# Kernel optimization log

Measured on AMD Instinct MI355X. Metric: run time of the kernel, lower is better.

## Reference

```python
import jax, jax.numpy as jnp
from jax import lax
import numpy as np

M, CLS, K, DL, DC, DO, BD = 87, 65, 128, 128, 128, 2048, 256
B, H, W = 256, 7, 7


def _c1(x, Wt, b):
    # 1x1 Conv2d: [B,Cin,H,W] -> [B,Cout,H,W]
    return jnp.einsum('oc,bchw->bohw', Wt, x) + b[None, :, None, None]


def _pagerank(edge, v_init, p=0.85, iters=100):
    # torch: transition = adj / adj.sum(dim=1)  (broadcast divides COLUMNS by row-sums)
    n = edge.shape[0]
    Wpr = p * edge / jnp.sum(edge, axis=1)[None, :]
    s = v_init * n                                  # [B,n,1]
    coef = (1.0 - p) / n
    def body(i, xv):
        zx = coef * jnp.sum(xv, axis=1, keepdims=True)      # z_T @ x -> [B,1,1]
        return jnp.einsum('ij,bjo->bio', Wpr, xv) + s * zx
    xv = lax.fori_loop(0, iters, body, s)
    nrm = jnp.sqrt(jnp.sum(xv * xv, axis=1, keepdims=True))  # F.normalize(dim=1)
    xv = xv / jnp.maximum(nrm, 1e-12)
    return (v_init + xv).reshape(v_init.shape[0], -1)        # [B,n]


def setup_inputs() -> dict:
    key = jax.random.key(0)
    ks = jax.random.split(key, 24)
    def w(k, shape, s=0.02):
        return jax.random.normal(k, shape, jnp.float32) * s
    rng = np.random.default_rng(0)
    A = (rng.random((M, M)) < 0.08).astype(np.float32)
    A = np.maximum(A, A.T)
    np.fill_diagonal(A, 1.0)   # symmetric adjacency with self-loops (degrees > 0)
    return {
        'x': jax.random.normal(ks[0], (B, DO, H, W), jnp.float32),
        'Wb': w(ks[1], (BD, DO)), 'bb': w(ks[2], (BD,), 0.01),
        'Wfc': w(ks[3], (CLS, BD)), 'Wfc2': w(ks[4], (CLS, BD)),
        'Wo1': w(ks[5], (4 * DL, DO)), 'bo1': w(ks[6], (4 * DL,), 0.01),
        'Wo2': w(ks[7], (DL, 4 * DL)), 'bo2': w(ks[8], (DL,), 0.01),
        'Wa': w(ks[9], (M, DL)), 'ba': w(ks[10], (M,), 0.01),
        'Wps': w(ks[11], (DC, DL)), 'bps': w(ks[12], (DC,), 0.01),
        'node_p': jax.random.uniform(ks[13], (K, M), jnp.float32, -0.1, 0.1),
        'Wg': w(ks[14], (DC, DC + K)), 'bg': w(ks[15], (DC,), 0.01),
        'Wsp': w(ks[16], (DL, DC)), 'bsp': w(ks[17], (DL,), 0.01),
        'Ws': w(ks[18], (1, DC + DL)), 'bs': w(ks[19], (1,), 0.01),
        'Wox1': w(ks[20], (4 * DL, DL)), 'box1': w(ks[21], (4 * DL,), 0.01),
        'Wox2': w(ks[22], (DO, 4 * DL)), 'box2': w(ks[23], (DO,), 0.01),
        'edge': jnp.asarray(A),
    }


def reference(x, Wb, bb, Wfc, Wfc2, Wo1, bo1, Wo2, bo2, Wa, ba, Wps, bps,
              node_p, Wg, bg, Wsp, bsp, Ws, bs, Wox1, box1, Wox2, box2, edge):
    Bsz, _, hl, wl = x.shape
    HW = hl * wl

    # global pooled branch
    x_p = jnp.mean(x, axis=(2, 3))                           # [B,2048]
    features_p = x_p @ Wb.T + bb                             # [B,256]
    pre_output = features_p @ Wfc.T                          # [B,65]
    pre_score = jax.nn.softmax(lax.stop_gradient(pre_output), axis=1)

    # personalized pagerank over the semantic graph (constant wrt grads)
    v_init = jnp.concatenate(
        [jnp.zeros((Bsz, M - CLS), x.dtype), pre_score], axis=1)[:, :, None]
    v_y = lax.stop_gradient(_pagerank(edge, v_init))         # [B,87]

    # local feature reduction 2048 -> 512 -> 128
    x_l = _c1(_c1(x, Wo1, bo1), Wo2, bo2)                    # [B,128,7,7]

    a = _c1(x_l, Wa, ba).reshape(Bsz, M, HW).transpose(0, 2, 1)   # [B,HW,87]
    ps = _c1(x_l, Wps, bps).reshape(Bsz, DC, HW)                  # [B,128,HW]
    m1 = jax.nn.relu(jnp.matmul(ps, a))                           # [B,128,87]

    # replicate torch's exact (k, B*m) reshape + flat v_y broadcast
    node = jnp.broadcast_to(node_p[None], (Bsz, K, M)).reshape(K, Bsz * M)
    node = (v_y.reshape(-1) * node).reshape(Bsz, K, M)

    g = jnp.einsum('oc,bcm->bom', Wg, jnp.concatenate([node, m1], axis=1)) \
        + bg[None, :, None]                                   # [B,128,87]

    # D^-1/2 A D^-1/2 graph propagation
    Dinv = jnp.sum(edge, axis=0) ** -0.5
    edge_norm = Dinv[:, None] * edge * Dinv[None, :]
    m2 = jax.nn.relu(jnp.einsum('bcm,mn->bcn', g, edge_norm))  # [B,128,87]

    sp = jnp.einsum('oc,bcm->bom', Wsp, m2) + bsp[None, :, None]  # [B,128,87]

    # conv_s over concat(m2_expand, x_expand) is separable: avoid the
    # [B,256,HW,87] tensor entirely (1 output channel, 1x1 kernel).
    Ws1, Ws2 = Ws[0, :DC], Ws[0, DC:]
    t_node = jnp.einsum('c,bcm->bm', Ws1, m2)                  # [B,87]
    t_pix = jnp.einsum('c,bcp->bp', Ws2, x_l.reshape(Bsz, DL, HW))  # [B,HW]
    s_logits = t_node[:, :, None] + t_pix[:, None, :] + bs[0]  # [B,87,HW]
    s_att = jax.nn.softmax(s_logits, axis=1)                   # softmax over nodes

    m3 = jax.nn.relu(jnp.matmul(sp, s_att)).reshape(Bsz, DL, hl, wl)
    m3 = _c1(_c1(m3, Wox1, box1), Wox2, box2)                  # [B,2048,7,7]

    feature_aug = jnp.mean(m3, axis=(2, 3)) @ Wb.T + bb
    features = features_p + feature_aug
    outputs2 = features @ Wfc2.T
    softmax_outputs = jax.nn.softmax(outputs2, axis=1)
    return (features, outputs2, softmax_outputs, pre_output, features_p)
```

## Files before the change

### kernel.cpp

```cpp
#include <hip/hip_runtime.h>
#include <cmath>


typedef __attribute__((ext_vector_type(8))) short short8;
typedef __attribute__((ext_vector_type(4))) short s16x4;
typedef __attribute__((ext_vector_type(4))) float f32x4;

constexpr size_t OFF_W12BF = 0;
constexpr size_t OFF_T1BF  = 131072;
constexpr size_t OFF_WBBF  = 262144;
constexpr size_t OFF_XPBF  = 524288;
constexpr size_t OFF_WAPBF = 786432;
constexpr size_t OFF_WG2BF = 800768;
constexpr size_t OFF_ENPBF = 808960;
constexpr size_t OFF_B215  = 813568;
constexpr size_t OFF_B12   = 813792;
constexpr size_t OFF_WPR   = 813920;
constexpr size_t OFF_BTMP  = 821496;
constexpr size_t OFF_WC    = 823544;
constexpr size_t OFF_BC    = 856312;
constexpr size_t OFF_VY    = 856568;
constexpr size_t OFF_NT    = 878848;
constexpr size_t OFF_PART  = 901376;

__device__ __forceinline__ unsigned short f2bf(float f) {
  unsigned u = __builtin_bit_cast(unsigned, f);
  u += 0x7fffu + ((u >> 16) & 1u);
  return (unsigned short)(u >> 16);
}
__device__ __forceinline__ float bf2f(unsigned short s) {
  return __builtin_bit_cast(float, ((unsigned)s) << 16);
}

__global__ __launch_bounds__(256) void ksetup_all(
    const float* __restrict__ Wb,  const float* __restrict__ bb,
    const float* __restrict__ Wa,  const float* __restrict__ ba,
    const float* __restrict__ Wps, const float* __restrict__ bps,
    const float* __restrict__ Wg,  const float* __restrict__ edge,
    const float* __restrict__ Wo2, const float* __restrict__ Wo1,
    const float* __restrict__ Wox2,const float* __restrict__ Wox1,
    const float* __restrict__ box1,const float* __restrict__ box2,
    const float* __restrict__ bo1, const float* __restrict__ bo2,
    float* __restrict__ ws, float* __restrict__ featp)
{
  __shared__ alignas(16) short As[64*72];
  __shared__ alignas(16) short Bs[64*72];
  int blk = blockIdx.x, tid = threadIdx.x;
  if (blk < 2048) {
    int idx = blk*256 + tid;
    ((unsigned short*)(ws+OFF_WBBF))[idx] = f2bf(Wb[idx]);
  } else if (blk < 2304) {
    int idx = (blk-2048)*256 + tid;
    featp[idx] = bb[idx & 255];
  } else if (blk < 2432) {
    int idx = (blk-2304)*256 + tid;
    ws[OFF_WC + idx] = 0.f;
  } else if (blk < 2544) {
    int idx = (blk-2432)*256 + tid;
    int r = idx >> 7, c = idx & 127;
    float v;
    if (r < 128)      v = Wps[r*128 + c];
    else if (r < 215) v = Wa[(r-128)*128 + c];
    else              v = 0.f;
    ((unsigned short*)(ws+OFF_WAPBF))[idx] = f2bf(v);
  } else if (blk < 2608) {
    int idx = (blk-2544)*256 + tid;
    int o = idx >> 7, d = idx & 127;
    ((unsigned short*)(ws+OFF_WG2BF))[idx] = f2bf(Wg[o*256 + 128 + d]);
  } else if (blk < 2644) {
    int idx = (blk-2608)*256 + tid;
    int m = idx / 96, n = idx % 96;
    float v = 0.f;
    if (m < 87 && n < 87) {
      float sm = 0.f, sn = 0.f;
      for (int k = 0; k < 87; ++k) { sm += edge[k*87+m]; sn += edge[k*87+n]; }
      v = edge[m*87+n] / sqrtf(sm*sn);
    }
    ((unsigned short*)(ws+OFF_ENPBF))[idx] = f2bf(v);
  } else if (blk < 2674) {
    int idx = (blk-2644)*256 + tid;
    if (idx < 87*87) {
      int j = idx % 87;
      float rs = 0.f;
      for (int k = 0; k < 87; ++k) rs += edge[j*87+k];
      ws[OFF_WPR + idx] = 0.85f * edge[idx] / rs;
    }
  } else if (blk == 2674) {
    if (tid < 224) {
      float v = (tid < 128) ? bps[tid] : (tid < 215 ? ba[tid-128] : 0.f);
      ws[OFF_B215 + tid] = v;
    }
  } else if (blk < 2803) {
    int gb = blk - 2675;
    const float *A, *B; unsigned short* C; int lda, ldb, ldc, i0, j0;
    if (gb < 64) {
      A = Wo2; B = Wo1; C = (unsigned short*)(ws+OFF_W12BF);
      lda = 512; ldb = 2048; ldc = 2048;
      i0 = (gb & 1)*64; j0 = (gb >> 1)*64;
    } else {
      int b2 = gb - 64;
      A = Wox2; B = Wox1; C = (unsigned short*)(ws+OFF_T1BF);
      lda = 512; ldb = 128; ldc = 128;
      i0 = (b2 >> 1)*64; j0 = (b2 & 1)*64;
    }
    int w = tid >> 6, l = tid & 63, quad = l >> 4, lane16 = l & 15;
    f32x4 acc[4];
    #pragma unroll
    for (int i = 0; i < 4; ++i) acc[i] = (f32x4)(0.f);
    for (int kc = 0; kc < 512; kc += 64) {
      for (int t = tid; t < 1024; t += 256) {
        int r = t >> 4, k4 = t & 15;
        float4 v = *(const float4*)&A[(size_t)(i0+r)*lda + kc + k4*4];
        s16x4 sv; sv[0]=(short)f2bf(v.x); sv[1]=(short)f2bf(v.y); sv[2]=(short)f2bf(v.z); sv[3]=(short)f2bf(v.w);
        *(s16x4*)&As[r*72 + k4*4] = sv;
      }
      for (int t = tid; t < 1024; t += 256) {
        int kr = t >> 4, n4 = t & 15;
        float4 v = *(const float4*)&B[(size_t)(kc+kr)*ldb + j0 + n4*4];
        Bs[(n4*4+0)*72 + kr] = (short)f2bf(v.x);
        Bs[(n4*4+1)*72 + kr] = (short)f2bf(v.y);
        Bs[(n4*4+2)*72 + kr] = (short)f2bf(v.z);
        Bs[(n4*4+3)*72 + kr] = (short)f2bf(v.w);
      }
      __syncthreads();
      #pragma unroll
      for (int ks = 0; ks < 2; ++ks) {
        short8 a = *(const short8*)&As[(w*16+lane16)*72 + ks*32 + quad*8];
        #pragma unroll
        for (int nt = 0; nt < 4; ++nt) {
          short8 b8 = *(const short8*)&Bs[(nt*16+lane16)*72 + ks*32 + quad*8];
          acc[nt] = __builtin_amdgcn_mfma_f32_16x16x32_bf16(a, b8, acc[nt], 0, 0, 0);
        }
      }
      __syncthreads();
    }
    #pragma unroll
    for (int nt = 0; nt < 4; ++nt)
      #pragma unroll
      for (int r = 0; r < 4; ++r)
        C[(size_t)(i0 + w*16 + quad*4 + r)*ldc + j0 + nt*16 + lane16] = f2bf(acc[nt][r]);
  } else {
    int vb = blk - 2803;
    int w = tid >> 6, l = tid & 63;
    if (vb < 512) {
      int o = vb*4 + w;
      float s = 0.f;
      for (int h = l; h < 512; h += 64) s += Wox2[(size_t)o*512 + h] * box1[h];
      for (int off = 32; off; off >>= 1) s += __shfl_down(s, off, 64);
      if (l == 0) ws[OFF_BTMP + o] = s + box2[o];
    } else {
      int o = (vb - 512)*4 + w;
      float s = 0.f;
      for (int h = l; h < 512; h += 64) s += Wo2[(size_t)o*512 + h] * bo1[h];
      for (int off = 32; off; off >>= 1) s += __shfl_down(s, off, 64);
      if (l == 0) ws[OFF_B12 + o] = s + bo2[o];
    }
  }
}

__global__ __launch_bounds__(256) void kwcbc(const float* __restrict__ Wb,
                                             const float* __restrict__ bb,
                                             float* __restrict__ ws)
{
  __shared__ alignas(16) short As[64*72];
  __shared__ alignas(16) short Bs[64*72];
  int blk = blockIdx.x, tid = threadIdx.x;
  if (blk < 64) {
    const short* wbbf = (const short*)(ws+OFF_WBBF);
    const short* t1s  = (const short*)(ws+OFF_T1BF);
    int i0 = (blk & 3)*64, j0 = ((blk >> 2) & 1)*64, kc0 = (blk >> 3)*256;
    int w = tid >> 6, l = tid & 63, quad = l >> 4, lane16 = l & 15;
    f32x4 acc[4];
    #pragma unroll
    for (int i = 0; i < 4; ++i) acc[i] = (f32x4)(0.f);
    for (int kc = kc0; kc < kc0+256; kc += 64) {
      for (int t = tid; t < 512; t += 256) {
        int r = t >> 3, c8 = t & 7;
        *(short8*)&As[r*72 + c8*8] = *(const short8*)&wbbf[(size_t)(i0+r)*2048 + kc + c8*8];
      }
      for (int t = tid; t < 1024; t += 256) {
        int kr = t >> 4, n4 = t & 15;
        s16x4 v = *(const s16x4*)&t1s[(size_t)(kc+kr)*128 + j0 + n4*4];
        Bs[(n4*4+0)*72 + kr] = v[0];
        Bs[(n4*4+1)*72 + kr] = v[1];
        Bs[(n4*4+2)*72 + kr] = v[2];
        Bs[(n4*4+3)*72 + kr] = v[3];
      }
      __syncthreads();
      #pragma unroll
      for (int ks = 0; ks < 2; ++ks) {
        short8 a = *(const short8*)&As[(w*16+lane16)*72 + ks*32 + quad*8];
        #pragma unroll
        for (int nt = 0; nt < 4; ++nt) {
          short8 b8 = *(const short8*)&Bs[(nt*16+lane16)*72 + ks*32 + quad*8];
          acc[nt] = __builtin_amdgcn_mfma_f32_16x16x32_bf16(a, b8, acc[nt], 0, 0, 0);
        }
      }
      __syncthreads();
    }
    #pragma unroll
    for (int nt = 0; nt < 4; ++nt)
      #pragma unroll
      for (int r = 0; r < 4; ++r)
        atomicAdd(&ws[OFF_WC + (size_t)(i0 + w*16 + quad*4 + r)*128 + j0 + nt*16 + lane16], acc[nt][r]);
  } else {
    int j = (blk-64)*4 + (tid >> 6), l = tid & 63;
    float s = 0.f;
    for (int c = l; c < 2048; c += 64) s += Wb[(size_t)j*2048 + c] * ws[OFF_BTMP + c];
    for (int off = 32; off; off >>= 1) s += __shfl_down(s, off, 64);
    if (l == 0) ws[OFF_BC + j] = s + bb[j];
  }
}

__global__ __launch_bounds__(512) void kmain4(const float* __restrict__ x,
                                              const short* __restrict__ w12bf,
                                              short* __restrict__ xpbf,
                                              float* __restrict__ part)
{
  __shared__ alignas(16) short Bt[2][52*72];
  int b = blockIdx.x, half = blockIdx.y, tid = threadIdx.x;
  int w = tid >> 6, l = tid & 63;
  int quad = l >> 4, lane16 = l & 15;
  const float* xb = x + ((size_t)b*2048 + half*1024)*49;

  int p0 = tid % 49, oct0 = tid / 49;
  bool has0 = (tid < 392);

  float g0[8];
  if (has0) {
    #pragma unroll
    for (int j = 0; j < 8; ++j) g0[j] = xb[(size_t)(oct0*8+j)*49 + p0];
  }

  f32x4 acc[4];
  #pragma unroll
  for (int i = 0; i < 4; ++i) acc[i] = (f32x4)(0.f);

  for (int kci = 0; kci < 16; ++kci) {
    int kc = kci*64;
    short* bt = Bt[kci & 1];
    if (has0) {
      short8 v;
      #pragma unroll
      for (int j = 0; j < 8; ++j) v[j] = (short)f2bf(g0[j]);
      *(short8*)(bt + p0*72 + oct0*8) = v;
    }
    __syncthreads();
    if (kci < 15 && has0) {
      const float* xc = xb + (size_t)(kc+64)*49;
      #pragma unroll
      for (int j = 0; j < 8; ++j) g0[j] = xc[(size_t)(oct0*8+j)*49 + p0];
    }
    const short* wr = w12bf + (size_t)(w*16 + lane16)*2048 + half*1024 + kc + quad*8;
    short8 a0 = *(const short8*)(wr);
    short8 a1 = *(const short8*)(wr + 32);
    #pragma unroll
    for (int ni = 0; ni < 4; ++ni) {
      const short* br = bt + (ni*16 + lane16)*72 + quad*8;
      short8 b0 = *(const short8*)(br);
      short8 b1 = *(const short8*)(br + 32);
      acc[ni] = __builtin_amdgcn_mfma_f32_16x16x32_bf16(a0, b0, acc[ni], 0, 0, 0);
      acc[ni] = __builtin_amdgcn_mfma_f32_16x16x32_bf16(a1, b1, acc[ni], 0, 0, 0);
    }
    if (tid < 64) {
      float s = 0.f;
      for (int p = 0; p < 49; ++p)
        s += bf2f((unsigned short)bt[p*72 + tid]);
      xpbf[(size_t)b*2048 + half*1024 + kc + tid] = (short)f2bf(s * (1.f/49.f));
    }
  }
  float* po = part + ((size_t)half*256 + b)*128*52;
  #pragma unroll
  for (int ni = 0; ni < 4; ++ni) {
    int p = ni*16 + lane16;
    if (p < 49) {
      #pragma unroll
      for (int r = 0; r < 4; ++r) {
        int o = w*16 + quad*4 + r;
        po[o*52 + p] = acc[ni][r];
      }
    }
  }
}

__global__ __launch_bounds__(256) void kfeat(const short* __restrict__ xpbf,
                                             const short* __restrict__ wbbf,
                                             float* __restrict__ featp)
{
  int i0 = blockIdx.x*64, j0 = blockIdx.y*64, kc0 = blockIdx.z*256;
  int tid = threadIdx.x, w = tid >> 6, l = tid & 63, quad = l >> 4, lane16 = l & 15;
  f32x4 acc[4];
  #pragma unroll
  for (int i = 0; i < 4; ++i) acc[i] = (f32x4)(0.f);
  for (int kc = kc0; kc < kc0+256; kc += 32) {
    short8 a = *(const short8*)&xpbf[(size_t)(i0 + w*16 + lane16)*2048 + kc + quad*8];
    #pragma unroll
    for (int nt = 0; nt < 4; ++nt) {
      short8 b8 = *(const short8*)&wbbf[(size_t)(j0 + nt*16 + lane16)*2048 + kc + quad*8];
      acc[nt] = __builtin_amdgcn_mfma_f32_16x16x32_bf16(a, b8, acc[nt], 0, 0, 0);
    }
  }
  #pragma unroll
  for (int nt = 0; nt < 4; ++nt)
    #pragma unroll
    for (int r = 0; r < 4; ++r)
      atomicAdd(&featp[(size_t)(i0 + w*16 + quad*4 + r)*256 + j0 + nt*16 + lane16], acc[nt][r]);
}

__global__ __launch_bounds__(128, 1) void kpr(const float* __restrict__ featp,
                                              const float* __restrict__ Wfc,
                                              const float* __restrict__ wpr,
                                              float* __restrict__ preo,
                                              float* __restrict__ vy)
{
  __shared__ alignas(16) float fpr[256];
  __shared__ alignas(16) float po[68];
  __shared__ alignas(16) float vs[2][88];
  __shared__ float red[2];
  int b = blockIdx.x, tid = threadIdx.x;
  fpr[tid] = featp[b*256 + tid];
  fpr[tid+128] = featp[b*256 + 128 + tid];
  __syncthreads();
  if (tid < 65) {
    float s = 0.f;
    for (int c = 0; c < 256; c += 4) {
      float4 w4 = *(const float4*)&Wfc[tid*256 + c];
      s += w4.x*fpr[c] + w4.y*fpr[c+1] + w4.z*fpr[c+2] + w4.w*fpr[c+3];
    }
    po[tid] = s;
    preo[b*65 + tid] = s;
  }
  __syncthreads();
  if (tid < 64) {
    float v = po[tid];
    if (tid == 0) v = fmaxf(v, po[64]);
    float mx = v;
    #pragma unroll
    for (int off = 32; off; off >>= 1) mx = fmaxf(mx, __shfl_down(mx, off, 64));
    mx = __shfl(mx, 0, 64);
    float e = expf(po[tid]-mx) + ((tid == 0) ? expf(po[64]-mx) : 0.f);
    float sm = e;
    #pragma unroll
    for (int off = 32; off; off >>= 1) sm += __shfl_down(sm, off, 64);
    if (tid == 0) { red[0] = mx; red[1] = 1.f/sm; }
  }
  __syncthreads();
  float vinit = 0.f;
  if (tid >= 22 && tid < 87) vinit = expf(po[tid-22]-red[0]) * red[1];
  float s_i = vinit * 87.f;
  float wrow[87];
  if (tid < 87) {
    float add = s_i * (0.15f/87.0f);
    #pragma unroll
    for (int j = 0; j < 87; ++j) wrow[j] = wpr[tid*87 + j] + add;
    vs[0][tid] = s_i;
  }
  __syncthreads();
  for (int it = 0; it < 64; ++it) {
    const float* vc = vs[it & 1];
    if (tid < 87) {
      float nv = 0.f;
      #pragma unroll
      for (int j4 = 0; j4 < 21; ++j4) {
        float4 v4 = *(const float4*)&vc[j4*4];
        nv += wrow[j4*4+0]*v4.x + wrow[j4*4+1]*v4.y + wrow[j4*4+2]*v4.z + wrow[j4*4+3]*v4.w;
      }
      nv += wrow[84]*vc[84] + wrow[85]*vc[85] + wrow[86]*vc[86];
      vs[(it+1) & 1][tid] = nv;
    }
    __syncthreads();
  }
  if (tid < 64) {
    float v = vs[0][tid]*vs[0][tid];
    if (tid < 23) v += vs[0][64+tid]*vs[0][64+tid];
    #pragma unroll
    for (int off = 32; off; off >>= 1) v += __shfl_down(v, off, 64);
    if (tid == 0) red[0] = 1.f / fmaxf(sqrtf(v), 1e-12f);
  }
  __syncthreads();
  if (tid < 87) vy[b*87 + tid] = vinit + vs[0][tid]*red[0];
}

__global__ __launch_bounds__(256) void knode(const float* __restrict__ Wg,
                                             const float* __restrict__ node_p,
                                             const float* __restrict__ vy,
                                             float* __restrict__ nt)
{
  int idx = blockIdx.x*256 + threadIdx.x;
  int par = idx / 11264;
  int r = idx % 11264;
  int o = r / 88, m = r % 88;
  float v = 0.f;
  if (m < 87) {
    float s = 0.f;
    for (int k = 0; k < 128; ++k)
      s += Wg[o*256+k] * node_p[k*87+m] * vy[(par*128+k)*87+m];
    v = s;
  }
  nt[idx] = v;
}

__global__ __launch_bounds__(512) void kgraph_all(
    const float* __restrict__ part,  const float* __restrict__ b12,
    const short* __restrict__ wapbf, const float* __restrict__ b215,
    const short* __restrict__ wg2bf, const float* __restrict__ nt,
    const float* __restrict__ bg,    const short* __restrict__ enpbf,
    const float* __restrict__ Wsp,   const float* __restrict__ bsp,
    const float* __restrict__ Ws,    const float* __restrict__ wc,
    const float* __restrict__ bc,    const float* __restrict__ featp,
    const float* __restrict__ Wfc2,
    float* __restrict__ feat, float* __restrict__ out2, float* __restrict__ soft)
{
  extern __shared__ char smraw[];
  short* XT = (short*)smraw;
  short* At = XT + 8704;
  short* M1 = At + 16128;
  short* G  = M1 + 13056;
  short* M2 = G  + 13312;
  float* fb  = (float*)(M2 + 13312);
  float* wsm = fb;
  float* tnb = fb + 96;
  float* zs  = fb + 192;
  float* m3s = fb + 320;
  float* fs  = fb + 448;
  float* o2s = fb + 704;
  float* red = fb + 776;

  int b = blockIdx.x, tid = threadIdx.x;
  int w = tid >> 6, l = tid & 63, quad = l >> 4, lane16 = l & 15;

  const float* pa = part + (size_t)b*128*52;
  const float* pb = pa + (size_t)256*128*52;
  for (int t = tid; t < 6656; t += 512) {
    int o = t / 52, p = t % 52;
    XT[p*136 + o] = (short)f2bf(pa[t] + pb[t] + b12[o]);
  }
  for (int t = tid; t < 1536; t += 512) {
    int p = 52 + t/128, o = t % 128;
    XT[p*136 + o] = 0;
  }
  __syncthreads();

  for (int t = w; t < 56; t += 8) {
    int mt = t >> 2, n4 = t & 3;
    f32x4 acc = (f32x4)(0.f);
    #pragma unroll
    for (int ks = 0; ks < 4; ++ks) {
      short8 a  = *(const short8*)&wapbf[(size_t)(mt*16+lane16)*128 + ks*32 + quad*8];
      short8 b8 = *(const short8*)&XT[(n4*16+lane16)*136 + ks*32 + quad*8];
      acc = __builtin_amdgcn_mfma_f32_16x16x32_bf16(a, b8, acc, 0, 0, 0);
    }
    int p = n4*16 + lane16;
    #pragma unroll
    for (int r = 0; r < 4; ++r) {
      int rr = mt*16 + quad*4 + r;
      At[rr*72 + p] = (p < 49) ? (short)f2bf(acc[r] + b215[rr]) : (short)0;
    }
  }
  __syncthreads();

  for (int t = w; t < 48; t += 8) {
    int mt = t / 8, n4 = t % 8;
    f32x4 acc = (f32x4)(0.f);
    #pragma unroll
    for (int ks = 0; ks < 2; ++ks) {
      short8 a  = *(const short8*)&At[(128 + mt*16 + lane16)*72 + ks*32 + quad*8];
      short8 b8 = *(const short8*)&At[(n4*16+lane16)*72 + ks*32 + quad*8];
      acc = __builtin_amdgcn_mfma_f32_16x16x32_bf16(a, b8, acc, 0, 0, 0);
    }
    int d = n4*16 + lane16;
    #pragma unroll
    for (int r = 0; r < 4; ++r) {
      int m = mt*16 + quad*4 + r;
      M1[m*136 + d] = (short)f2bf(fmaxf(acc[r], 0.f));
    }
  }
  __syncthreads();

  const float* ntb = nt + (size_t)(b & 1)*11264;
  for (int t = w; t < 48; t += 8) {
    int mt = t / 6, n4 = t % 6;
    f32x4 acc = (f32x4)(0.f);
    #pragma unroll
    for (int ks = 0; ks < 4; ++ks) {
      short8 a  = *(const short8*)&wg2bf[(size_t)(mt*16+lane16)*128 + ks*32 + quad*8];
      short8 b8 = *(const short8*)&M1[(n4*16+lane16)*136 + ks*32 + quad*8];
      acc = __builtin_amdgcn_mfma_f32_16x16x32_bf16(a, b8, acc, 0, 0, 0);
    }
    int m = n4*16 + lane16;
    #pragma unroll
    for (int r = 0; r < 4; ++r) {
      int o = mt*16 + quad*4 + r;
      float v = acc[r] + bg[o] + ((m < 88) ? ntb[o*88 + m] : 0.f);
      G[o*104 + m] = (short)f2bf(v);
    }
  }
  __syncthreads();

  for (int t = w; t < 48; t += 8) {
    int mt = t / 6, n4 = t % 6;
    f32x4 acc = (f32x4)(0.f);
    #pragma unroll
    for (int ks = 0; ks < 3; ++ks) {
      short8 a  = *(const short8*)&G[(mt*16+lane16)*104 + ks*32 + quad*8];
      short8 b8 = *(const short8*)&enpbf[(size_t)(n4*16+lane16)*96 + ks*32 + quad*8];
      acc = __builtin_amdgcn_mfma_f32_16x16x32_bf16(a, b8, acc, 0, 0, 0);
    }
    int n = n4*16 + lane16;
    #pragma unroll
    for (int r = 0; r < 4; ++r) {
      int c = mt*16 + quad*4 + r;
      M2[c*104 + n] = (short)f2bf(fmaxf(acc[r], 0.f));
    }
  }
  __syncthreads();

  if (tid < 87) {
    float s = 0.f;
    for (int c = 0; c < 128; ++c) s += Ws[c] * bf2f((unsigned short)M2[c*104 + tid]);
    tnb[tid] = s;
  }
  __syncthreads();
  if (tid < 64) {
    float v = tnb[tid];
    if (tid < 23) v = fmaxf(v, tnb[64+tid]);
    float mx = v;
    #pragma unroll
    for (int off = 32; off; off >>= 1) mx = fmaxf(mx, __shfl_down(mx, off, 64));
    mx = __shfl(mx, 0, 64);
    float e0 = expf(tnb[tid]-mx);
    float e1 = (tid < 23) ? expf(tnb[64+tid]-mx) : 0.f;
    float sm = e0 + e1;
    #pragma unroll
    for (int off = 32; off; off >>= 1) sm += __shfl_down(sm, off, 64);
    sm = __shfl(sm, 0, 64);
    float inv = 1.f/sm;
    wsm[tid] = e0*inv;
    if (tid < 23) wsm[64+tid] = e1*inv;
  }
  __syncthreads();
  if (tid < 128) {
    float s = 0.f;
    for (int m = 0; m < 87; ++m) s += bf2f((unsigned short)M2[tid*104 + m]) * wsm[m];
    zs[tid] = s;
  }
  __syncthreads();
  if (tid < 128) {
    float s = 0.f;
    for (int c = 0; c < 128; ++c) s += Wsp[tid*128 + c] * zs[c];
    m3s[tid] = fmaxf(s + bsp[tid], 0.f);
  }
  __syncthreads();

  if (tid < 256) {
    float s = 0.f;
    #pragma unroll 4
    for (int d4 = 0; d4 < 32; ++d4) {
      float4 w4 = *(const float4*)&wc[tid*128 + d4*4];
      s += w4.x*m3s[d4*4] + w4.y*m3s[d4*4+1] + w4.z*m3s[d4*4+2] + w4.w*m3s[d4*4+3];
    }
    float f = featp[b*256 + tid] + bc[tid] + s;
    fs[tid] = f;
    feat[b*256 + tid] = f;
  }
  __syncthreads();
  if (tid < 65) {
    float s = 0.f;
    for (int j = 0; j < 256; ++j) s += Wfc2[tid*256 + j] * fs[j];
    out2[b*65 + tid] = s;
    o2s[tid] = s;
  }
  __syncthreads();
  if (tid < 64) {
    float v = o2s[tid];
    if (tid == 0) v = fmaxf(v, o2s[64]);
    float mx = v;
    #pragma unroll
    for (int off = 32; off; off >>= 1) mx = fmaxf(mx, __shfl_down(mx, off, 64));
    mx = __shfl(mx, 0, 64);
    float e = expf(o2s[tid]-mx) + ((tid == 0) ? expf(o2s[64]-mx) : 0.f);
    float sm = e;
    #pragma unroll
    for (int off = 32; off; off >>= 1) sm += __shfl_down(sm, off, 64);
    if (tid == 0) { red[0] = mx; red[1] = 1.f/sm; }
  }
  __syncthreads();
  if (tid < 65) soft[b*65 + tid] = expf(o2s[tid]-red[0]) * red[1];
}

extern "C" void kernel_launch(void* const* d_in, const int* in_sizes, int n_in,
                              void* d_out, int out_size, void* d_ws, size_t ws_size,
                              hipStream_t stream)
{
  (void)in_sizes; (void)n_in; (void)out_size; (void)ws_size;
  const float* x      = (const float*)d_in[0];
  const float* Wb     = (const float*)d_in[1];
  const float* bb     = (const float*)d_in[2];
  const float* Wfc    = (const float*)d_in[3];
  const float* Wfc2   = (const float*)d_in[4];
  const float* Wo1    = (const float*)d_in[5];
  const float* bo1    = (const float*)d_in[6];
  const float* Wo2    = (const float*)d_in[7];
  const float* bo2    = (const float*)d_in[8];
  const float* Wa     = (const float*)d_in[9];
  const float* ba     = (const float*)d_in[10];
  const float* Wps    = (const float*)d_in[11];
  const float* bps    = (const float*)d_in[12];
  const float* node_p = (const float*)d_in[13];
  const float* Wg     = (const float*)d_in[14];
  const float* bg     = (const float*)d_in[15];
  const float* Wsp    = (const float*)d_in[16];
  const float* bsp    = (const float*)d_in[17];
  const float* Ws     = (const float*)d_in[18];
  const float* Wox1   = (const float*)d_in[20];
  const float* box1   = (const float*)d_in[21];
  const float* Wox2   = (const float*)d_in[22];
  const float* box2   = (const float*)d_in[23];
  const float* edge   = (const float*)d_in[24];

  float* ws   = (float*)d_ws;
  float* out  = (float*)d_out;
  float* feat  = out;
  float* out2  = out + 65536;
  float* soft  = out + 82176;
  float* preo  = out + 98816;
  float* featp = out + 115456;

  ksetup_all<<<3347, 256, 0, stream>>>(Wb, bb, Wa, ba, Wps, bps, Wg, edge,
                                       Wo2, Wo1, Wox2, Wox1, box1, box2, bo1, bo2,
                                       ws, featp);
  kwcbc<<<128, 256, 0, stream>>>(Wb, bb, ws);
  kmain4<<<dim3(256,2), 512, 0, stream>>>(x, (const short*)(ws + OFF_W12BF),
                                          (short*)(ws + OFF_XPBF), ws + OFF_PART);
  kfeat<<<dim3(4,4,8), 256, 0, stream>>>((const short*)(ws + OFF_XPBF),
                                         (const short*)(ws + OFF_WBBF), featp);
  kpr<<<256, 128, 0, stream>>>(featp, Wfc, ws + OFF_WPR, preo, ws + OFF_VY);
  knode<<<88, 256, 0, stream>>>(Wg, node_p, ws + OFF_VY, ws + OFF_NT);
  kgraph_all<<<256, 512, 132144, stream>>>(ws + OFF_PART, ws + OFF_B12,
                                           (const short*)(ws + OFF_WAPBF),
                                           ws + OFF_B215,
                                           (const short*)(ws + OFF_WG2BF),
                                           ws + OFF_NT, bg,
                                           (const short*)(ws + OFF_ENPBF),
                                           Wsp, bsp, Ws,
                                           ws + OFF_WC, ws + OFF_BC, featp, Wfc2,
                                           feat, out2, soft);
}
```

Before: 369.9 us.

## Split main GEMM four ways over channels and fuse feature GEMM into the weight-prep kernel

The main 1x1-conv GEMM kernel now splits the 2048-channel reduction into four quarters instead of two, launching 1024 blocks with fewer K iterations each. The input tile is loaded with float4 vector reads and written transposed into shared memory. kgraph_all now sums four partial buffers instead of two. The separate kfeat launch is merged into the kwcbc kernel as extra blocks, which removes one launch. The cost is twice as much partial-sum storage and traffic, scalar shared-memory stores that may bank-conflict, and unaligned float4 loads.

New measurement: 362.6 us. 2.0% less time.

```diff
diff --git a/kernel.cpp b/kernel.cpp
--- a/kernel.cpp
+++ b/kernel.cpp
@@ -158,9 +158,103 @@
   }
 }
 
-__global__ __launch_bounds__(256) void kwcbc(const float* __restrict__ Wb,
-                                             const float* __restrict__ bb,
-                                             float* __restrict__ ws)
+__global__ __launch_bounds__(512, 6) void kmain5(const float* __restrict__ x,
+                                                 const short* __restrict__ w12bf,
+                                                 short* __restrict__ xpbf,
+                                                 float* __restrict__ part)
+{
+  __shared__ alignas(16) short Bt[2][64*72];
+  int b = blockIdx.x, q = blockIdx.y, tid = threadIdx.x;
+  int w = tid >> 6, l = tid & 63;
+  int quad = l >> 4, lane16 = l & 15;
+  const float* xb = x + ((size_t)b*2048 + q*512)*49;
+
+  int p4A = tid % 13, cA = tid / 13;
+  int tB = tid + 512;
+  int p4B = tB % 13, cB = tB / 13;
+  bool hasB = (tid < 320);
+
+  float fA[4], fB[4];
+  {
+    if (p4A < 12) {
+      float4 v = *(const float4*)(xb + cA*49 + p4A*4);
+      fA[0]=v.x; fA[1]=v.y; fA[2]=v.z; fA[3]=v.w;
+    } else fA[0] = xb[cA*49 + 48];
+    if (hasB) {
+      if (p4B < 12) {
+        float4 v = *(const float4*)(xb + cB*49 + p4B*4);
+        fB[0]=v.x; fB[1]=v.y; fB[2]=v.z; fB[3]=v.w;
+      } else fB[0] = xb[cB*49 + 48];
+    }
+  }
+
+  f32x4 acc[4];
+  #pragma unroll
+  for (int i = 0; i < 4; ++i) acc[i] = (f32x4)(0.f);
+
+  for (int kci = 0; kci < 8; ++kci) {
+    short* bt = Bt[kci & 1];
+    if (p4A < 12) {
+      #pragma unroll
+      for (int i = 0; i < 4; ++i) bt[(p4A*4+i)*72 + cA] = (short)f2bf(fA[i]);
+    } else bt[48*72 + cA] = (short)f2bf(fA[0]);
+    if (hasB) {
+      if (p4B < 12) {
+        #pragma unroll
+        for (int i = 0; i < 4; ++i) bt[(p4B*4+i)*72 + cB] = (short)f2bf(fB[i]);
+      } else bt[48*72 + cB] = (short)f2bf(fB[0]);
+    }
+    __syncthreads();
+    if (kci < 7) {
+      const float* xc = xb + (size_t)(kci+1)*64*49;
+      if (p4A < 12) {
+        float4 v = *(const float4*)(xc + cA*49 + p4A*4);
+        fA[0]=v.x; fA[1]=v.y; fA[2]=v.z; fA[3]=v.w;
+      } else fA[0] = xc[cA*49 + 48];
+      if (hasB) {
+        if (p4B < 12) {
+          float4 v = *(const float4*)(xc + cB*49 + p4B*4);
+          fB[0]=v.x; fB[1]=v.y; fB[2]=v.z; fB[3]=v.w;
+        } else fB[0] = xc[cB*49 + 48];
+      }
+    }
+    const short* wr = w12bf + (size_t)(w*16 + lane16)*2048 + q*512 + kci*64 + quad*8;
+    short8 a0 = *(const short8*)(wr);
+    short8 a1 = *(const short8*)(wr + 32);
+    #pragma unroll
+    for (int ni = 0; ni < 4; ++ni) {
+      const short* br = bt + (ni*16 + lane16)*72 + quad*8;
+      short8 b0 = *(const short8*)(br);
+      short8 b1 = *(const short8*)(br + 32);
+      acc[ni] = __builtin_amdgcn_mfma_f32_16x16x32_bf16(a0, b0, acc[ni], 0, 0, 0);
+      acc[ni] = __builtin_amdgcn_mfma_f32_16x16x32_bf16(a1, b1, acc[ni], 0, 0, 0);
+    }
+    if (tid < 64) {
+      float s = 0.f;
+      for (int p = 0; p < 49; ++p)
+        s += bf2f((unsigned short)bt[p*72 + tid]);
+      xpbf[(size_t)b*2048 + q*512 + kci*64 + tid] = (short)f2bf(s * (1.f/49.f));
+    }
+  }
+  float* po = part + ((size_t)q*256 + b)*6656;
+  #pragma unroll
+  for (int ni = 0; ni < 4; ++ni) {
+    int p = ni*16 + lane16;
+    if (p < 49) {
+      #pragma unroll
+      for (int r = 0; r < 4; ++r) {
+        int o = w*16 + quad*4 + r;
+        po[o*52 + p] = acc[ni][r];
+      }
+    }
+  }
+}
+
+__global__ __launch_bounds__(256) void kwcf(const float* __restrict__ Wb,
+                                            const float* __restrict__ bb,
+                                            const short* __restrict__ xpbf,
+                                            float* __restrict__ featp,
+                                            float* __restrict__ ws)
 {
   __shared__ alignas(16) short As[64*72];
   __shared__ alignas(16) short Bs[64*72];
@@ -203,108 +297,34 @@
       #pragma unroll
       for (int r = 0; r < 4; ++r)
         atomicAdd(&ws[OFF_WC + (size_t)(i0 + w*16 + quad*4 + r)*128 + j0 + nt*16 + lane16], acc[nt][r]);
-  } else {
+  } else if (blk < 128) {
     int j = (blk-64)*4 + (tid >> 6), l = tid & 63;
     float s = 0.f;
     for (int c = l; c < 2048; c += 64) s += Wb[(size_t)j*2048 + c] * ws[OFF_BTMP + c];
     for (int off = 32; off; off >>= 1) s += __shfl_down(s, off, 64);
     if (l == 0) ws[OFF_BC + j] = s + bb[j];
-  }
-}
-
-__global__ __launch_bounds__(512) void kmain4(const float* __restrict__ x,
-                                              const short* __restrict__ w12bf,
-                                              short* __restrict__ xpbf,
-                                              float* __restrict__ part)
-{
-  __shared__ alignas(16) short Bt[2][52*72];
-  int b = blockIdx.x, half = blockIdx.y, tid = threadIdx.x;
-  int w = tid >> 6, l = tid & 63;
-  int quad = l >> 4, lane16 = l & 15;
-  const float* xb = x + ((size_t)b*2048 + half*1024)*49;
-
-  int p0 = tid % 49, oct0 = tid / 49;
-  bool has0 = (tid < 392);
-
-  float g0[8];
-  if (has0) {
-    #pragma unroll
-    for (int j = 0; j < 8; ++j) g0[j] = xb[(size_t)(oct0*8+j)*49 + p0];
-  }
-
-  f32x4 acc[4];
-  #pragma unroll
-  for (int i = 0; i < 4; ++i) acc[i] = (f32x4)(0.f);
-
-  for (int kci = 0; kci < 16; ++kci) {
-    int kc = kci*64;
-    short* bt = Bt[kci & 1];
-    if (has0) {
-      short8 v;
-      #pragma unroll
-      for (int j = 0; j < 8; ++j) v[j] = (short)f2bf(g0[j]);
-      *(short8*)(bt + p0*72 + oct0*8) = v;
-    }
-    __syncthreads();
-    if (kci < 15 && has0) {
-      const float* xc = xb + (size_t)(kc+64)*49;
-      #pragma unroll
-      for (int j = 0; j < 8; ++j) g0[j] = xc[(size_t)(oct0*8+j)*49 + p0];
-    }
-    const short* wr = w12bf + (size_t)(w*16 + lane16)*2048 + half*1024 + kc + quad*8;
-    short8 a0 = *(const short8*)(wr);
-    short8 a1 = *(const short8*)(wr + 32);
-    #pragma unroll
-    for (int ni = 0; ni < 4; ++ni) {
-      const short* br = bt + (ni*16 + lane16)*72 + quad*8;
-      short8 b0 = *(const short8*)(br);
-      short8 b1 = *(const short8*)(br + 32);
-      acc[ni] = __builtin_amdgcn_mfma_f32_16x16x32_bf16(a0, b0, acc[ni], 0, 0, 0);
-      acc[ni] = __builtin_amdgcn_mfma_f32_16x16x32_bf16(a1, b1, acc[ni], 0, 0, 0);
-    }
-    if (tid < 64) {
-      float s = 0.f;
-      for (int p = 0; p < 49; ++p)
-        s += bf2f((unsigned short)bt[p*72 + tid]);
-      xpbf[(size_t)b*2048 + half*1024 + kc + tid] = (short)f2bf(s * (1.f/49.f));
-    }
-  }
-  float* po = part + ((size_t)half*256 + b)*128*52;
-  #pragma unroll
-  for (int ni = 0; ni < 4; ++ni) {
-    int p = ni*16 + lane16;
-    if (p < 49) {
-      #pragma unroll
-      for (int r = 0; r < 4; ++r) {
-        int o = w*16 + quad*4 + r;
-        po[o*52 + p] = acc[ni][r];
-      }
-    }
-  }
-}
-
-__global__ __launch_bounds__(256) void kfeat(const short* __restrict__ xpbf,
-                                             const short* __restrict__ wbbf,
-                                             float* __restrict__ featp)
-{
-  int i0 = blockIdx.x*64, j0 = blockIdx.y*64, kc0 = blockIdx.z*256;
-  int tid = threadIdx.x, w = tid >> 6, l = tid & 63, quad = l >> 4, lane16 = l & 15;
-  f32x4 acc[4];
-  #pragma unroll
-  for (int i = 0; i < 4; ++i) acc[i] = (f32x4)(0.f);
-  for (int kc = kc0; kc < kc0+256; kc += 32) {
-    short8 a = *(const short8*)&xpbf[(size_t)(i0 + w*16 + lane16)*2048 + kc + quad*8];
-    #pragma unroll
-    for (int nt = 0; nt < 4; ++nt) {
-      short8 b8 = *(const short8*)&wbbf[(size_t)(j0 + nt*16 + lane16)*2048 + kc + quad*8];
-      acc[nt] = __builtin_amdgcn_mfma_f32_16x16x32_bf16(a, b8, acc[nt], 0, 0, 0);
-    }
-  }
-  #pragma unroll
-  for (int nt = 0; nt < 4; ++nt)
-    #pragma unroll
-    for (int r = 0; r < 4; ++r)
-      atomicAdd(&featp[(size_t)(i0 + w*16 + quad*4 + r)*256 + j0 + nt*16 + lane16], acc[nt][r]);
+  } else {
+    const short* wbbf = (const short*)(ws+OFF_WBBF);
+    int idx = blk - 128;
+    int i0 = (idx & 3)*64, j0 = ((idx >> 2) & 3)*64, kc0 = (idx >> 4)*256;
+    int w = tid >> 6, l = tid & 63, quad = l >> 4, lane16 = l & 15;
+    f32x4 acc[4];
+    #pragma unroll
+    for (int i = 0; i < 4; ++i) acc[i] = (f32x4)(0.f);
+    for (int kc = kc0; kc < kc0+256; kc += 32) {
+      short8 a = *(const short8*)&xpbf[(size_t)(i0 + w*16 + lane16)*2048 + kc + quad*8];
+      #pragma unroll
+      for (int nt = 0; nt < 4; ++nt) {
+        short8 b8 = *(const short8*)&wbbf[(size_t)(j0 + nt*16 + lane16)*2048 + kc + quad*8];
+        acc[nt] = __builtin_amdgcn_mfma_f32_16x16x32_bf16(a, b8, acc[nt], 0, 0, 0);
+      }
+    }
+    #pragma unroll
+    for (int nt = 0; nt < 4; ++nt)
+      #pragma unroll
+      for (int r = 0; r < 4; ++r)
+        atomicAdd(&featp[(size_t)(i0 + w*16 + quad*4 + r)*256 + j0 + nt*16 + lane16], acc[nt][r]);
+  }
 }
 
 __global__ __launch_bounds__(128, 1) void kpr(const float* __restrict__ featp,
@@ -429,11 +449,13 @@
   int b = blockIdx.x, tid = threadIdx.x;
   int w = tid >> 6, l = tid & 63, quad = l >> 4, lane16 = l & 15;
 
-  const float* pa = part + (size_t)b*128*52;
-  const float* pb = pa + (size_t)256*128*52;
+  const float* p0 = part + (size_t)b*6656;
+  const float* p1 = p0 + (size_t)256*6656;
+  const float* p2 = p1 + (size_t)256*6656;
+  const float* p3 = p2 + (size_t)256*6656;
   for (int t = tid; t < 6656; t += 512) {
     int o = t / 52, p = t % 52;
-    XT[p*136 + o] = (short)f2bf(pa[t] + pb[t] + b12[o]);
+    XT[p*136 + o] = (short)f2bf(p0[t] + p1[t] + p2[t] + p3[t] + b12[o]);
   }
   for (int t = tid; t < 1536; t += 512) {
     int p = 52 + t/128, o = t % 128;
@@ -629,11 +651,9 @@
   ksetup_all<<<3347, 256, 0, stream>>>(Wb, bb, Wa, ba, Wps, bps, Wg, edge,
                                        Wo2, Wo1, Wox2, Wox1, box1, box2, bo1, bo2,
                                        ws, featp);
-  kwcbc<<<128, 256, 0, stream>>>(Wb, bb, ws);
-  kmain4<<<dim3(256,2), 512, 0, stream>>>(x, (const short*)(ws + OFF_W12BF),
+  kmain5<<<dim3(256,4), 512, 0, stream>>>(x, (const short*)(ws + OFF_W12BF),
                                           (short*)(ws + OFF_XPBF), ws + OFF_PART);
-  kfeat<<<dim3(4,4,8), 256, 0, stream>>>((const short*)(ws + OFF_XPBF),
-                                         (const short*)(ws + OFF_WBBF), featp);
+  kwcf<<<256, 256, 0, stream>>>(Wb, bb, (const short*)(ws + OFF_XPBF), featp, ws);
   kpr<<<256, 128, 0, stream>>>(featp, Wfc, ws + OFF_WPR, preo, ws + OFF_VY);
   knode<<<88, 256, 0, stream>>>(Wg, node_p, ws + OFF_VY, ws + OFF_NT);
   kgraph_all<<<256, 512, 132144, stream>>>(ws + OFF_PART, ws + OFF_B12,
```
